# Kernel tuning notes

Hardware: AMD Instinct MI355X
Metric: run time of the kernel (lower is better)

## Reference

```python
import jax, jax.numpy as jnp
import numpy as np

NUM_STEPS = 151
STEP = 2.0 / (NUM_STEPS - 1)
# mirror torch.arange(-1, 1 + step, step) to get the exact bin count
T_BINS = np.arange(-1.0, 1.0 + STEP, STEP)
TSIZE = len(T_BINS)


def setup_inputs() -> dict:
    key = jax.random.key(0)
    k1, k2 = jax.random.split(key)
    feats = jax.random.normal(k1, (8192, 256), dtype=jnp.float32)
    # embeddings must be L2-normalized so similarities lie in [-1, 1]
    feats = feats / jnp.linalg.norm(feats, axis=1, keepdims=True)
    classes = jax.random.randint(k2, (8192,), 0, 100, dtype=jnp.int64)
    return {"features": feats, "classes": classes}


def reference(features, classes):
    N = features.shape[0]
    dists = features @ features.T  # [N, N] cosine similarities
    iu, ju = jnp.triu_indices(N, k=1)  # static upper-triangular pair indices
    s = dists[iu, ju]                  # [P] pair similarities
    same = classes[iu] == classes[ju]  # [P] pos-pair mask

    # soft (linear-interpolation) histogram: the torch code builds O(tsize*P)
    # masks; the identical math is a scatter-add of (1-frac) to the lower bin
    # and frac to the upper bin. floor is detached in the original (.data),
    # and jnp.floor has zero gradient, so autodiff semantics match.
    f = jnp.floor(s / STEP) * STEP
    frac = (s - f) / STEP
    k_low = jnp.clip(jnp.round((f + 1.0) / STEP).astype(jnp.int32), 0, TSIZE - 1)
    k_up = jnp.clip(k_low + 1, 0, TSIZE - 1)

    def histogram(mask):
        w = mask.astype(s.dtype)
        h = jnp.zeros((TSIZE,), s.dtype)
        h = h.at[k_low].add(w * (1.0 - frac)).at[k_up].add(w * frac)
        size = jnp.maximum(mask.sum(), 1).astype(s.dtype)
        return h / size

    hist_pos = histogram(same)
    hist_neg = histogram(~same)
    # inclusive cumsum == tril-masked repeat + sum in the original
    cdf_pos = jnp.cumsum(hist_pos)
    return jnp.sum(hist_neg * cdf_pos)
```

## Files before the change

kernel.cpp:

```cpp
#include <hip/hip_runtime.h>


#define NN   8192
#define DD   256
#define BM   128
#define TS   151
#define NREP 8
#define NTILES 2080
#define NB   1024

typedef __attribute__((ext_vector_type(4))) float floatx4;

#define GLL16(g, l)                                                     \
    __builtin_amdgcn_global_load_lds(                                   \
        (const __attribute__((address_space(1))) void*)(g),             \
        (__attribute__((address_space(3))) void*)(l), 16, 0, 0)

__device__ __forceinline__ void decode_tile(int t, int& bi, int& bj) {
    int rem = t, b = 0;
    while (rem >= 64 - b) { rem -= 64 - b; ++b; }
    bi = b; bj = b + rem;
}

__global__ __launch_bounds__(256)
void split_f8(const float* __restrict__ F, unsigned char* __restrict__ f8B,
              unsigned long long* __restrict__ gacc ) {
    if (blockIdx.x == 0) {
        for (int i = threadIdx.x; i < 4 * TS; i += 256) gacc[i] = 0ull;
    }
    const int j = blockIdx.x * 256 + threadIdx.x;
    const int R = j >> 4, u = j & 15;
    const float* src = F + (size_t)R * DD + u * 16;
    const float4 v0 = *(const float4*)src;
    const float4 v1 = *(const float4*)(src + 4);
    const float4 v2 = *(const float4*)(src + 8);
    const float4 v3 = *(const float4*)(src + 12);
    uint4 w;
    {
        int t0 = __builtin_amdgcn_cvt_pk_fp8_f32(v0.x, v0.y, 0, false);
        w.x = (unsigned)__builtin_amdgcn_cvt_pk_fp8_f32(v0.z, v0.w, t0, true);
        int t1 = __builtin_amdgcn_cvt_pk_fp8_f32(v1.x, v1.y, 0, false);
        w.y = (unsigned)__builtin_amdgcn_cvt_pk_fp8_f32(v1.z, v1.w, t1, true);
        int t2 = __builtin_amdgcn_cvt_pk_fp8_f32(v2.x, v2.y, 0, false);
        w.z = (unsigned)__builtin_amdgcn_cvt_pk_fp8_f32(v2.z, v2.w, t2, true);
        int t3 = __builtin_amdgcn_cvt_pk_fp8_f32(v3.x, v3.y, 0, false);
        w.w = (unsigned)__builtin_amdgcn_cvt_pk_fp8_f32(v3.z, v3.w, t3, true);
    }
    const int pos = (u & ~1) | ((u & 1) ^ ((R >> 2) & 1));
    *(uint4*)(f8B + (size_t)R * 256 + pos * 16) = w;
}

__global__ __launch_bounds__(256, 4)
void gram_hist(const unsigned char* __restrict__ f8B,
               const int* __restrict__ cls,
               unsigned long long* __restrict__ glo,
               unsigned long long* __restrict__ ghi) {
    __shared__ __align__(16) unsigned char smem[16384];
    __shared__ __align__(16) unsigned long long hist_s[2 * NREP * TS];

    const int tid  = threadIdx.x;
    const int lane = tid & 63;
    const int wave = tid >> 6;
    const int wr = wave >> 1, wc = wave & 1;
    const int r = lane & 15;
    const int h = lane >> 4;
    const unsigned swz = ((((unsigned)h >> 1) ^ (((unsigned)r >> 2) & 1u)) << 4)
                       | (((unsigned)h & 1u) << 3);

    const int srow = lane >> 1;
    const int scolb = (lane & 1) * 16;
    const unsigned ldsb = (unsigned)wave * 1024;

#define STAGE(buf, kt, xA, xB)                                                \
    do {                                                                      \
        const unsigned ko_ = (unsigned)(kt) * 32;                             \
        const unsigned bb_ = (unsigned)(buf) * 8192;                          \
        GLL16(f8B + (xA) + ko_, smem + bb_ + ldsb);                           \
        GLL16(f8B + (xB) + ko_, smem + bb_ + 4096 + ldsb);                    \
    } while (0)

    for (int i = tid; i < 2 * NREP * TS; i += 256) hist_s[i] = 0ull;

    int t = (int)blockIdx.x;
    int bi, bj;
    decode_tile(t, bi, bj);
    int ibase = bi * BM, jbase = bj * BM;
    unsigned oA = (unsigned)(ibase + wave * 32 + srow) * 256 + scolb;
    unsigned oB = (unsigned)(jbase + wave * 32 + srow) * 256 + scolb;

    STAGE(0, 0, oA, oB);
    __syncthreads();

    const int rep = lane & (NREP - 1);
    unsigned long long* const hp0 = hist_s + rep * TS;
    unsigned long long* const hp1 = hp0 + NREP * TS;
    const float SC = 75.0f * 65536.0f;

    for (; t < NTILES; t += NB) {
        int ci[4][4], cj[4];
#pragma unroll
        for (int mi = 0; mi < 4; ++mi)
#pragma unroll
            for (int reg = 0; reg < 4; ++reg)
                ci[mi][reg] = cls[ibase + wr * 64 + mi * 16 + h * 4 + reg];
#pragma unroll
        for (int ni = 0; ni < 4; ++ni)
            cj[ni] = cls[jbase + wc * 64 + ni * 16 + r];

        floatx4 acc[4][4];
        const floatx4 zf = {0.f, 0.f, 0.f, 0.f};
#pragma unroll
        for (int mi = 0; mi < 4; ++mi)
#pragma unroll
            for (int ni = 0; ni < 4; ++ni) acc[mi][ni] = zf;

#pragma unroll
        for (int kt = 0; kt < DD / 32; ++kt) {
            const unsigned bb = (unsigned)(kt & 1) * 8192;
            if (kt < DD / 32 - 1)
                STAGE((kt & 1) ^ 1, kt + 1, oA, oB);

            unsigned long long Ah[4];
#pragma unroll
            for (int mi = 0; mi < 4; ++mi) {
                const unsigned o = (unsigned)(wr * 64 + mi * 16 + r) * 32 + swz;
                Ah[mi] = *(const unsigned long long*)(smem + bb + o);
            }
            __builtin_amdgcn_s_setprio(1);
#pragma unroll
            for (int ni = 0; ni < 4; ++ni) {
                const unsigned o = (unsigned)(wc * 64 + ni * 16 + r) * 32 + swz;
                const unsigned long long Bh = *(const unsigned long long*)(smem + bb + 4096 + o);
#pragma unroll
                for (int mi = 0; mi < 4; ++mi)
                    acc[mi][ni] = __builtin_amdgcn_mfma_f32_16x16x32_fp8_fp8(
                        (long long)Ah[mi], (long long)Bh, acc[mi][ni], 0, 0, 0);
            }
            __builtin_amdgcn_s_setprio(0);
            __syncthreads();
        }

        int nbi = bi, nbj = bj;
        unsigned nA = oA, nB = oB;
        if (t + NB < NTILES) {
            decode_tile(t + NB, nbi, nbj);
            nA = (unsigned)(nbi * BM + wave * 32 + srow) * 256 + scolb;
            nB = (unsigned)(nbj * BM + wave * 32 + srow) * 256 + scolb;
            STAGE(0, 0, nA, nB);
        }

#define BINLOOP(GUARDED)                                                      \
    _Pragma("unroll")                                                         \
    for (int mi = 0; mi < 4; ++mi)                                            \
        _Pragma("unroll")                                                     \
        for (int ni = 0; ni < 4; ++ni)                                        \
            _Pragma("unroll")                                                 \
            for (int reg = 0; reg < 4; ++reg) {                               \
                if (GUARDED) {                                                \
                    const int gi = ibase + wr * 64 + mi * 16 + h * 4 + reg;   \
                    const int gj = jbase + wc * 64 + ni * 16 + r;             \
                    if (gi >= gj) continue;                                   \
                }                                                             \
                int Yi = (int)fmaf(acc[mi][ni][reg], SC, SC);                 \
                Yi = min(max(Yi, 0), 150 * 65536);                            \
                const int k = Yi >> 16;                                       \
                const unsigned q = (unsigned)Yi & 65535u;                     \
                const unsigned long long val =                                \
                    ((unsigned long long)q << 32) | (unsigned long long)(65536u - q); \
                atomicAdd((ci[mi][reg] == cj[ni]) ? &hp0[k] : &hp1[k], val);  \
            }

        if (bi != bj) { BINLOOP(false) } else { BINLOOP(true) }
#undef BINLOOP

        bi = nbi; bj = nbj;
        ibase = bi * BM; jbase = bj * BM;
        oA = nA; oB = nB;

        __syncthreads();
    }
#undef STAGE

    for (int i = tid; i < 2 * TS; i += 256) {
        const int p = i / TS, b = i - p * TS;
        unsigned long long s = 0;
#pragma unroll
        for (int r2 = 0; r2 < NREP; ++r2) s += hist_s[(p * NREP + r2) * TS + b];
        const unsigned long long lo = s & 0xFFFFFFFFull;
        const unsigned long long hi = s >> 32;
        if (lo) atomicAdd(&glo[i], lo);
        if (hi) atomicAdd(&ghi[i], hi);
    }
}

__global__ __launch_bounds__(256)
void finalize_loss(const unsigned long long* __restrict__ glo,
                   const unsigned long long* __restrict__ ghi,
                   float* __restrict__ out) {
    __shared__ double smp[TS], smn[TS];
    const int tid = threadIdx.x;
    for (int b = tid; b < TS; b += 256) {
        smp[b] = (double)glo[b]      + (b ? (double)ghi[b - 1]      : 0.0);
        smn[b] = (double)glo[TS + b] + (b ? (double)ghi[TS + b - 1] : 0.0);
    }
    __syncthreads();
    if (tid == 0) {
        double posmass = 0.0;
        for (int b = 0; b < TS; ++b) posmass += smp[b];
        const double P = 33550336.0;
        double cpos = posmass * (1.0 / 65536.0);
        double cneg = P - cpos;
        if (cpos < 1.0) cpos = 1.0;
        if (cneg < 1.0) cneg = 1.0;
        const double inv_np = 1.0 / (65536.0 * cpos);
        const double inv_nn = 1.0 / (65536.0 * cneg);
        double cdf = 0.0, loss = 0.0;
        for (int b = 0; b < TS; ++b) {
            cdf  += smp[b] * inv_np;
            loss += smn[b] * cdf;
        }
        out[0] = (float)(loss * inv_nn);
    }
}

#define ROWB 80
#define NREPF 8
typedef __attribute__((ext_vector_type(8))) short short8;

__device__ __forceinline__ unsigned int bf16_rtne(float x) {
    unsigned int u = __builtin_bit_cast(unsigned int, x);
    return (u + 0x7FFFu + ((u >> 16) & 1u)) >> 16;
}
__device__ __forceinline__ void split_store_fb(unsigned char* hi_p, unsigned char* lo_p, float4 v) {
    unsigned ax = __builtin_bit_cast(unsigned, v.x), ay = __builtin_bit_cast(unsigned, v.y);
    unsigned az = __builtin_bit_cast(unsigned, v.z), aw = __builtin_bit_cast(unsigned, v.w);
    uint2 hi; hi.x = (ax >> 16) | (ay & 0xFFFF0000u); hi.y = (az >> 16) | (aw & 0xFFFF0000u);
    float lx = v.x - __builtin_bit_cast(float, ax & 0xFFFF0000u);
    float ly = v.y - __builtin_bit_cast(float, ay & 0xFFFF0000u);
    float lz = v.z - __builtin_bit_cast(float, az & 0xFFFF0000u);
    float lw = v.w - __builtin_bit_cast(float, aw & 0xFFFF0000u);
    uint2 lo; lo.x = bf16_rtne(lx) | (bf16_rtne(ly) << 16); lo.y = bf16_rtne(lz) | (bf16_rtne(lw) << 16);
    *(uint2*)hi_p = hi; *(uint2*)lo_p = lo;
}

__global__ __launch_bounds__(256, 2)
void gram_hist_fb(const float* __restrict__ F, const int* __restrict__ cls,
                  unsigned long long* __restrict__ ghist, unsigned int* __restrict__ gposcnt) {
    __shared__ unsigned char smem[4 * BM * ROWB];
    __shared__ unsigned int s_pos;
    const int tid = threadIdx.x, lane = tid & 63, wave = tid >> 6;
    const int wr = wave >> 1, wc = wave & 1, r = lane & 15, h = lane >> 4;
    const int T = NN / BM;
    int rem = (int)blockIdx.x; int bi = 0;
    while (rem >= T - bi) { rem -= T - bi; ++bi; }
    const int bj = bi + rem, ibase = bi * BM, jbase = bj * BM;
    const unsigned AHI = 0, ALO = BM * ROWB, BHI = 2 * BM * ROWB, BLO = 3 * BM * ROWB;
    floatx4 acc[4][4]; const floatx4 zf = {0.f,0.f,0.f,0.f};
    for (int mi = 0; mi < 4; ++mi) for (int ni = 0; ni < 4; ++ni) acc[mi][ni] = zf;
    for (int kt = 0; kt < DD / 32; ++kt) {
        const int k0 = kt * 32;
        __syncthreads();
        for (int t = 0; t < 4; ++t) {
            const int idx = tid + t * 256, row = idx >> 3, q = idx & 7;
            const unsigned off = (unsigned)row * ROWB + (unsigned)q * 8;
            split_store_fb(smem + AHI + off, smem + ALO + off,
                           *(const float4*)(F + (size_t)(ibase + row) * DD + k0 + q * 4));
            split_store_fb(smem + BHI + off, smem + BLO + off,
                           *(const float4*)(F + (size_t)(jbase + row) * DD + k0 + q * 4));
        }
        __syncthreads();
        short8 Ah[4], Al[4];
        for (int mi = 0; mi < 4; ++mi) {
            const unsigned o = (unsigned)(wr * 64 + mi * 16 + r) * ROWB + (unsigned)h * 16;
            Ah[mi] = *(const short8*)(smem + AHI + o); Al[mi] = *(const short8*)(smem + ALO + o);
        }
        for (int ni = 0; ni < 4; ++ni) {
            const unsigned o = (unsigned)(wc * 64 + ni * 16 + r) * ROWB + (unsigned)h * 16;
            const short8 Bh = *(const short8*)(smem + BHI + o);
            const short8 Bl = *(const short8*)(smem + BLO + o);
            for (int mi = 0; mi < 4; ++mi) {
                acc[mi][ni] = __builtin_amdgcn_mfma_f32_16x16x32_bf16(Ah[mi], Bh, acc[mi][ni], 0, 0, 0);
                acc[mi][ni] = __builtin_amdgcn_mfma_f32_16x16x32_bf16(Ah[mi], Bl, acc[mi][ni], 0, 0, 0);
                acc[mi][ni] = __builtin_amdgcn_mfma_f32_16x16x32_bf16(Al[mi], Bh, acc[mi][ni], 0, 0, 0);
            }
        }
    }
    __syncthreads();
    unsigned int* hist = (unsigned int*)smem;
    for (int i = tid; i < 2 * NREPF * TS; i += 256) hist[i] = 0u;
    if (tid == 0) s_pos = 0u;
    __syncthreads();
    int ci[4][4], cj[4];
    for (int mi = 0; mi < 4; ++mi) for (int reg = 0; reg < 4; ++reg)
        ci[mi][reg] = cls[ibase + wr * 64 + mi * 16 + h * 4 + reg];
    for (int ni = 0; ni < 4; ++ni) cj[ni] = cls[jbase + wc * 64 + ni * 16 + r];
    const bool offdiag = (bi != bj); const int rep = lane & (NREPF - 1);
    unsigned int cpos = 0;
    for (int mi = 0; mi < 4; ++mi) for (int ni = 0; ni < 4; ++ni) for (int reg = 0; reg < 4; ++reg) {
        const int gi = ibase + wr * 64 + mi * 16 + h * 4 + reg;
        const int gj = jbase + wc * 64 + ni * 16 + r;
        if (offdiag || gi < gj) {
            int Yi = (int)fmaf(acc[mi][ni][reg], 75.0f * 65536.0f, 75.0f * 65536.0f);
            Yi = min(max(Yi, 0), 150 * 65536);
            const int k = Yi >> 16; const unsigned q = (unsigned)Yi & 65535u;
            const int ku = min(k + 1, TS - 1);
            const int p = (ci[mi][reg] == cj[ni]) ? 0 : 1;
            cpos += (p == 0) ? 1u : 0u;
            atomicAdd(&hist[(p * NREPF + rep) * TS + k], 65536u - q);
            atomicAdd(&hist[(p * NREPF + rep) * TS + ku], q);
        }
    }
    atomicAdd(&s_pos, cpos);
    __syncthreads();
    for (int i = tid; i < 2 * TS; i += 256) {
        unsigned long long sum = 0;
        for (int r2 = 0; r2 < NREPF; ++r2) sum += hist[((i / TS) * NREPF + r2) * TS + (i % TS)];
        if (sum) atomicAdd(&ghist[i], sum);
    }
    if (tid == 0 && s_pos) atomicAdd(gposcnt, s_pos);
}

__global__ void finalize_fb(const unsigned long long* __restrict__ ghist,
                            const unsigned int* __restrict__ gposcnt, float* __restrict__ out) {
    if (threadIdx.x == 0 && blockIdx.x == 0) {
        const double P = 33550336.0, SCALE = 65536.0;
        double cpos = (double)(*gposcnt), cneg = P - cpos;
        if (cpos < 1.0) cpos = 1.0; if (cneg < 1.0) cneg = 1.0;
        double cdf = 0.0, loss = 0.0;
        for (int b = 0; b < TS; ++b) {
            cdf  += (double)ghist[b] / (SCALE * cpos);
            loss += ((double)ghist[TS + b] / (SCALE * cneg)) * cdf;
        }
        out[0] = (float)loss;
    }
}

extern "C" void kernel_launch(void* const* d_in, const int* in_sizes, int n_in,
                              void* d_out, int out_size, void* d_ws, size_t ws_size,
                              hipStream_t stream) {
    const float* F = (const float*)d_in[0];
    const int* cls = (const int*)d_in[1];

    const size_t FQ = (size_t)NN * DD;
    const size_t need = FQ + 4 * TS * sizeof(unsigned long long) + 64;

    if (ws_size >= need) {
        unsigned char* f8 = (unsigned char*)d_ws;
        unsigned long long* glo = (unsigned long long*)((char*)d_ws + FQ);
        unsigned long long* ghi = glo + 2 * TS;
        split_f8<<<dim3(NN * DD / 16 / 256), dim3(256), 0, stream>>>(F, f8, glo);
        gram_hist<<<dim3(NB), dim3(256), 0, stream>>>(f8, cls, glo, ghi);
        finalize_loss<<<1, 256, 0, stream>>>(glo, ghi, (float*)d_out);
    } else {
        unsigned long long* ghist = (unsigned long long*)d_ws;
        unsigned int* gcnt = (unsigned int*)((char*)d_ws + 2 * TS * sizeof(unsigned long long));
        hipMemsetAsync(d_ws, 0, 2 * TS * sizeof(unsigned long long) + sizeof(unsigned int), stream);
        gram_hist_fb<<<dim3(NTILES), dim3(256), 0, stream>>>(F, cls, ghist, gcnt);
        finalize_fb<<<1, 64, 0, stream>>>(ghist, gcnt, (float*)d_out);
    }
}
```

Before: 66.37 us.

## Use atomic tile queue, fuse finalize into last block, change LDS swizzle

```diff
diff --git a/kernel.cpp b/kernel.cpp
--- a/kernel.cpp
+++ b/kernel.cpp
@@ -24,9 +24,11 @@
 
 __global__ __launch_bounds__(256)
 void split_f8(const float* __restrict__ F, unsigned char* __restrict__ f8B,
-              unsigned long long* __restrict__ gacc ) {
+              unsigned long long* __restrict__ gacc ,
+              unsigned int* __restrict__ ctr ) {
     if (blockIdx.x == 0) {
         for (int i = threadIdx.x; i < 4 * TS; i += 256) gacc[i] = 0ull;
+        if (threadIdx.x == 0) { ctr[0] = NB; ctr[1] = 0u; }
     }
     const int j = blockIdx.x * 256 + threadIdx.x;
     const int R = j >> 4, u = j & 15;
@@ -35,28 +37,35 @@
     const float4 v1 = *(const float4*)(src + 4);
     const float4 v2 = *(const float4*)(src + 8);
     const float4 v3 = *(const float4*)(src + 12);
-    uint4 w;
+    unsigned g0, g1, g2, g3;
     {
         int t0 = __builtin_amdgcn_cvt_pk_fp8_f32(v0.x, v0.y, 0, false);
-        w.x = (unsigned)__builtin_amdgcn_cvt_pk_fp8_f32(v0.z, v0.w, t0, true);
+        g0 = (unsigned)__builtin_amdgcn_cvt_pk_fp8_f32(v0.z, v0.w, t0, true);
         int t1 = __builtin_amdgcn_cvt_pk_fp8_f32(v1.x, v1.y, 0, false);
-        w.y = (unsigned)__builtin_amdgcn_cvt_pk_fp8_f32(v1.z, v1.w, t1, true);
+        g1 = (unsigned)__builtin_amdgcn_cvt_pk_fp8_f32(v1.z, v1.w, t1, true);
         int t2 = __builtin_amdgcn_cvt_pk_fp8_f32(v2.x, v2.y, 0, false);
-        w.z = (unsigned)__builtin_amdgcn_cvt_pk_fp8_f32(v2.z, v2.w, t2, true);
+        g2 = (unsigned)__builtin_amdgcn_cvt_pk_fp8_f32(v2.z, v2.w, t2, true);
         int t3 = __builtin_amdgcn_cvt_pk_fp8_f32(v3.x, v3.y, 0, false);
-        w.w = (unsigned)__builtin_amdgcn_cvt_pk_fp8_f32(v3.z, v3.w, t3, true);
-    }
-    const int pos = (u & ~1) | ((u & 1) ^ ((R >> 2) & 1));
-    *(uint4*)(f8B + (size_t)R * 256 + pos * 16) = w;
+        g3 = (unsigned)__builtin_amdgcn_cvt_pk_fp8_f32(v3.z, v3.w, t3, true);
+    }
+    const int x = (R >> 2) & 3;
+    const int u2 = u ^ (x >> 1);
+    uint4 w;
+    if (x & 1) { w.x = g2; w.y = g3; w.z = g0; w.w = g1; }
+    else       { w.x = g0; w.y = g1; w.z = g2; w.w = g3; }
+    *(uint4*)(f8B + (size_t)R * 256 + u2 * 16) = w;
 }
 
 __global__ __launch_bounds__(256, 4)
 void gram_hist(const unsigned char* __restrict__ f8B,
                const int* __restrict__ cls,
                unsigned long long* __restrict__ glo,
-               unsigned long long* __restrict__ ghi) {
+               unsigned long long* __restrict__ ghi,
+               unsigned int* __restrict__ ctr,
+               float* __restrict__ out) {
     __shared__ __align__(16) unsigned char smem[16384];
     __shared__ __align__(16) unsigned long long hist_s[2 * NREP * TS];
+    __shared__ int s_next;
 
     const int tid  = threadIdx.x;
     const int lane = tid & 63;
@@ -64,8 +73,7 @@
     const int wr = wave >> 1, wc = wave & 1;
     const int r = lane & 15;
     const int h = lane >> 4;
-    const unsigned swz = ((((unsigned)h >> 1) ^ (((unsigned)r >> 2) & 1u)) << 4)
-                       | (((unsigned)h & 1u) << 3);
+    const unsigned swz = (unsigned)((h ^ (r >> 2)) & 3) << 3;
 
     const int srow = lane >> 1;
     const int scolb = (lane & 1) * 16;
@@ -96,7 +104,9 @@
     unsigned long long* const hp1 = hp0 + NREP * TS;
     const float SC = 75.0f * 65536.0f;
 
-    for (; t < NTILES; t += NB) {
+    while (true) {
+        if (tid == 0) s_next = (int)atomicAdd(&ctr[0], 1u);
+
         int ci[4][4], cj[4];
 #pragma unroll
         for (int mi = 0; mi < 4; ++mi)
@@ -140,10 +150,11 @@
             __syncthreads();
         }
 
+        const int tn = s_next;
         int nbi = bi, nbj = bj;
         unsigned nA = oA, nB = oB;
-        if (t + NB < NTILES) {
-            decode_tile(t + NB, nbi, nbj);
+        if (tn < NTILES) {
+            decode_tile(tn, nbi, nbj);
             nA = (unsigned)(nbi * BM + wave * 32 + srow) * 256 + scolb;
             nB = (unsigned)(nbj * BM + wave * 32 + srow) * 256 + scolb;
             STAGE(0, 0, nA, nB);
@@ -173,11 +184,11 @@
         if (bi != bj) { BINLOOP(false) } else { BINLOOP(true) }
 #undef BINLOOP
 
+        __syncthreads();
+        if (tn >= NTILES) break;
         bi = nbi; bj = nbj;
         ibase = bi * BM; jbase = bj * BM;
         oA = nA; oB = nB;
-
-        __syncthreads();
     }
 #undef STAGE
 
@@ -191,17 +202,21 @@
         if (lo) atomicAdd(&glo[i], lo);
         if (hi) atomicAdd(&ghi[i], hi);
     }
-}
-
-__global__ __launch_bounds__(256)
-void finalize_loss(const unsigned long long* __restrict__ glo,
-                   const unsigned long long* __restrict__ ghi,
-                   float* __restrict__ out) {
-    __shared__ double smp[TS], smn[TS];
-    const int tid = threadIdx.x;
+
+    __threadfence();
+    if (tid == 0) s_next = (int)atomicAdd(&ctr[1], 1u);
+    __syncthreads();
+    if (s_next != NB - 1) return;
+
+    double* smp = (double*)hist_s;
+    double* smn = smp + TS;
     for (int b = tid; b < TS; b += 256) {
-        smp[b] = (double)glo[b]      + (b ? (double)ghi[b - 1]      : 0.0);
-        smn[b] = (double)glo[TS + b] + (b ? (double)ghi[TS + b - 1] : 0.0);
+        const double plo = (double)atomicAdd(&glo[b], 0ull);
+        const double phi = b ? (double)atomicAdd(&ghi[b - 1], 0ull) : 0.0;
+        const double nlo = (double)atomicAdd(&glo[TS + b], 0ull);
+        const double nhi = b ? (double)atomicAdd(&ghi[TS + b - 1], 0ull) : 0.0;
+        smp[b] = plo + phi;
+        smn[b] = nlo + nhi;
     }
     __syncthreads();
     if (tid == 0) {
@@ -342,15 +357,15 @@
     const int* cls = (const int*)d_in[1];
 
     const size_t FQ = (size_t)NN * DD;
-    const size_t need = FQ + 4 * TS * sizeof(unsigned long long) + 64;
+    const size_t need = FQ + 4 * TS * sizeof(unsigned long long) + 2 * sizeof(unsigned int) + 64;
 
     if (ws_size >= need) {
         unsigned char* f8 = (unsigned char*)d_ws;
         unsigned long long* glo = (unsigned long long*)((char*)d_ws + FQ);
         unsigned long long* ghi = glo + 2 * TS;
-        split_f8<<<dim3(NN * DD / 16 / 256), dim3(256), 0, stream>>>(F, f8, glo);
-        gram_hist<<<dim3(NB), dim3(256), 0, stream>>>(f8, cls, glo, ghi);
-        finalize_loss<<<1, 256, 0, stream>>>(glo, ghi, (float*)d_out);
+        unsigned int* ctr = (unsigned int*)(ghi + 2 * TS);
+        split_f8<<<dim3(NN * DD / 16 / 256), dim3(256), 0, stream>>>(F, f8, glo, ctr);
+        gram_hist<<<dim3(NB), dim3(256), 0, stream>>>(f8, cls, glo, ghi, ctr, (float*)d_out);
     } else {
         unsigned long long* ghist = (unsigned long long*)d_ws;
         unsigned int* gcnt = (unsigned int*)((char*)d_ws + 2 * TS * sizeof(unsigned long long));
```

New measurement: 115.9 us. 74.7% more time.
